# Optimization experiments

Measured on AMD Instinct MI355X. Metric: run time of the kernel, lower is better.

The kernel has to match this reference:

```python
import jax, jax.numpy as jnp
import numpy as np

M1, M2, BS = 2000, 400, 8
AT = M1 + M2
E1, E2, E3 = 60000, 20000, 20000
H, F, NG, L, C = 64, 64, 50, 4, 4
CUTOFF = 10.0
LOG2 = 0.6931471805599453  # shift of ShiftedSoftplus


def _ssp(x):
    return jax.nn.softplus(x) - LOG2


def _smear(d):
    # GaussianSmearing(0, cutoff, NG)
    offset = jnp.linspace(0.0, CUTOFF, NG)
    coeff = -0.5 / (offset[1] - offset[0]) ** 2
    return jnp.exp(coeff * (d[:, None] - offset[None, :]) ** 2)  # [E, NG]


def _colored_mlp(attr, colors, w1, b1, w2, b2):
    # w1:[C,NG,F] b1:[C,F] w2:[C,F,F] b2:[C,F]; route each edge through its color's MLP
    out = jnp.zeros((attr.shape[0], w1.shape[-1]), attr.dtype)
    for c in range(C):  # fixed small color count
        h = _ssp(attr @ w1[c] + b1[c]) @ w2[c] + b2[c]
        out = out + jnp.where((colors == c)[:, None], h, jnp.zeros((), attr.dtype))
    return out


def _block(h, ei, ew, attr, col, p):
    # InteractionBlock: CFConv -> ssp -> linear
    mw1, mb1, mw2, mb2, cw1, cw2, cb2, bw, bb = p
    Ccut = 0.5 * (jnp.cos(ew * jnp.pi / CUTOFF) + 1.0)
    W = _colored_mlp(attr, col, mw1, mb1, mw2, mb2) * Ccut[:, None]  # [E,F]
    x = h @ cw1                                   # lin1 (no bias) [N,F]
    msg = x[ei[:, 0]] * W                         # gather x_j, modulate
    agg = jax.ops.segment_sum(msg, ei[:, 1], num_segments=h.shape[0])  # scatter-add
    x = agg @ cw2 + cb2                           # lin2
    return _ssp(x) @ bw + bb                      # act + block linear


def _batch_graph(ei, ew, col):
    # replicate per-structure edges across the batch with node offset b*AT
    offs = (jnp.arange(BS, dtype=ei.dtype) * AT)[:, None, None]
    ei_b = (ei[None] + offs).reshape(-1, 2)
    return ei_b, jnp.tile(ew, BS), jnp.tile(col, BS)


def _forward(sites, sites_p, e1, ew1, c1, e2, ew2, c2, e3, ew3, c3,
             emb_w, emb_p_w, mlp_w1, mlp_b1, mlp_w2, mlp_b2,
             conv_w1, conv_w2, conv_b2, blk_w, blk_b,
             out_w1, out_b1, out_w2, out_b2):
    h = jnp.concatenate([emb_w[sites], emb_p_w[sites_p]], axis=1).reshape(BS * AT, H)
    graphs = []
    for (ei, ew, col) in ((e1, ew1, c1), (e2, ew2, c2), (e3, ew3, c3)):
        ei_b, ew_b, col_b = _batch_graph(ei, ew, col)
        graphs.append((ei_b, ew_b, col_b, _smear(ew_b)))
    for l in range(L):
        delta = jnp.zeros_like(h)
        for g, (ei_b, ew_b, col_b, attr_b) in enumerate(graphs):
            p = (mlp_w1[l, g], mlp_b1[l, g], mlp_w2[l, g], mlp_b2[l, g],
                 conv_w1[l, g], conv_w2[l, g], conv_b2[l, g], blk_w[l, g], blk_b[l, g])
            delta = delta + _block(h, ei_b, ew_b, attr_b, col_b, p)
        h = h + delta
    hp = h.reshape(BS, AT, H)[:, M1:, :]   # mask selects pore nodes only
    o = hp @ out_w1 + out_b1               # NB: original has `h - self.act(h)` no-op, so no activation here
    o = o @ out_w2 + out_b2                # [BS, M2, 1]
    return o.sum(axis=1)                   # 'add' readout per batch -> [BS, 1]


def setup_inputs() -> dict:
    key = jax.random.key(0)
    ks = jax.random.split(key, 24)
    f = lambda i, shape, s=0.1: jax.random.normal(ks[i], shape, jnp.float32) * s
    sites = jax.random.randint(ks[0], (BS, M1), 0, 1, dtype=jnp.int32)
    sites_p = jax.random.randint(ks[1], (BS, M2), 0, 2, dtype=jnp.int32)
    e1 = jax.random.randint(ks[2], (E1, 2), 0, M1, dtype=jnp.int32)
    e2 = jnp.stack([jax.random.randint(ks[3], (E2,), 0, M1, dtype=jnp.int32),
                    jax.random.randint(ks[4], (E2,), M1, AT, dtype=jnp.int32)], 1)
    e3 = jnp.stack([jax.random.randint(ks[5], (E3,), M1, AT, dtype=jnp.int32),
                    jax.random.randint(ks[6], (E3,), 0, M1, dtype=jnp.int32)], 1)
    ew1 = jax.random.uniform(ks[7], (E1,), jnp.float32, 0.5, CUTOFF)
    ew2 = jax.random.uniform(ks[8], (E2,), jnp.float32, 0.5, CUTOFF)
    ew3 = jax.random.uniform(ks[9], (E3,), jnp.float32, 0.5, CUTOFF)
    c1 = jax.random.randint(ks[10], (E1,), 0, C, dtype=jnp.int32)
    c2 = jax.random.randint(ks[11], (E2,), 0, C, dtype=jnp.int32)
    c3 = jax.random.randint(ks[12], (E3,), 0, C, dtype=jnp.int32)
    return {
        'sites': sites, 'sites_p': sites_p,
        'edge_idx1': e1, 'edge_weight1': ew1, 'colors1': c1,
        'edge_idx2': e2, 'edge_weight2': ew2, 'colors2': c2,
        'edge_idx3': e3, 'edge_weight3': ew3, 'colors3': c3,
        'emb_w': f(13, (1, H), 1.0), 'emb_p_w': f(14, (2, H), 1.0),
        'mlp_w1': f(15, (L, 3, C, NG, F)), 'mlp_b1': jnp.zeros((L, 3, C, F), jnp.float32),
        'mlp_w2': f(16, (L, 3, C, F, F)), 'mlp_b2': jnp.zeros((L, 3, C, F), jnp.float32),
        'conv_w1': f(17, (L, 3, H, F)), 'conv_w2': f(18, (L, 3, F, H)),
        'conv_b2': jnp.zeros((L, 3, H), jnp.float32),
        'blk_w': f(19, (L, 3, H, H)), 'blk_b': jnp.zeros((L, 3, H), jnp.float32),
        'out_w1': f(20, (H, H // 2)), 'out_b1': jnp.zeros((H // 2,), jnp.float32),
        'out_w2': f(21, (H // 2, 1)), 'out_b2': jnp.zeros((1,), jnp.float32),
    }


def reference(sites, sites_p, edge_idx1, edge_weight1, colors1,
              edge_idx2, edge_weight2, colors2, edge_idx3, edge_weight3, colors3,
              emb_w, emb_p_w, mlp_w1, mlp_b1, mlp_w2, mlp_b2,
              conv_w1, conv_w2, conv_b2, blk_w, blk_b,
              out_w1, out_b1, out_w2, out_b2):
    return _forward(sites, sites_p, edge_idx1, edge_weight1, colors1,
                    edge_idx2, edge_weight2, colors2, edge_idx3, edge_weight3, colors3,
                    emb_w, emb_p_w, mlp_w1, mlp_b1, mlp_w2, mlp_b2,
                    conv_w1, conv_w2, conv_b2, blk_w, blk_b,
                    out_w1, out_b1, out_w2, out_b2)
```

## Files before the change

### kernel.cpp

```cpp
#include <hip/hip_runtime.h>
#include <math.h>

constexpr int M1 = 2000, M2 = 400, BS = 8;
constexpr int AT = M1 + M2;
constexpr int NN = BS * AT;
constexpr int E1 = 60000, E2 = 20000, E3 = 20000;
constexpr int ET = E1 + E2 + E3;
constexpr int H = 64, F = 64, NG = 50, L = 4, C = 4;
constexpr float CUTOFF = 10.0f;
constexpr float LOG2F_ = 0.6931471805599453f;

constexpr float SMEAR_STEP = 10.0f / 49.0f;
constexpr float SMEAR_COEFF = -12.005f;
constexpr float PI_OVER_CUT = 0.31415926535897932f;

constexpr int NBLK = (ET + 255) / 256;

constexpr int NT = 256;
constexpr float DSCALE = (float)(NT - 1) / CUTOFF;

constexpr int TILE_M = 32;

constexpr int SITE_T = M1 / 4;
constexpr int PORE_T = M2 / 4;
constexpr int NTILE  = SITE_T + PORE_T;

constexpr int LT0 = M1 / 4;
constexpr int LT1 = M1 / 4;
constexpr int LT2 = M2 / 4;
constexpr int LTOT = LT0 + LT1 + LT2;

constexpr int A_TAB  = 48 * NT / 4;
constexpr int A_INIT = NN * 64 / 256;
constexpr int A_CNT  = NBLK;
constexpr int A_CV   = 3;
constexpr int A_TOT  = A_TAB + A_INIT + A_CNT + A_CV;
constexpr int B_PACK = 48 * NT * 64 / 256;
constexpr int B_TOT  = B_PACK + 3 + 2;

constexpr size_t O_HA    = 0;
constexpr size_t O_HB    = O_HA  + (size_t)NN * 64 * 4;
constexpr size_t O_XG    = O_HB  + (size_t)NN * 64 * 4;
constexpr size_t O_DG    = O_XG  + (size_t)3 * AT * 512 * 2;
constexpr size_t O_TAB2  = O_DG  + (size_t)3 * NN * 64 * 4;
constexpr size_t O_EDATA = O_TAB2 + (size_t)48 * NT * 64 * 4;
constexpr size_t O_INT   = O_EDATA + (size_t)ET * 16;
constexpr int I_DEG  = 0;
constexpr int I_CUR  = 7200;
constexpr int I_ZEND = 14400;
constexpr int I_BASE = 14400;
constexpr int I_PERM = 21616;
constexpr int I_CV   = 26016;

__device__ inline float sspf(float x) {
    return fmaxf(x, 0.0f) + log1pf(expf(-fabsf(x))) - LOG2F_;
}
__device__ inline float sspf_fast(float x) {
    float t = __expf(-fabsf(x));
    return fmaxf(x, 0.0f) + __logf(1.0f + t) - LOG2F_;
}

__device__ inline unsigned int bf16rn(float x) {
    unsigned int u = __float_as_uint(x);
    u = (u + 0x7FFFu + ((u >> 16) & 1u)) >> 16;
    return u & 0xFFFFu;
}

__device__ inline int graph_off(int g) { return g == 0 ? 0 : (g == 1 ? E1 : E1 + E2); }

__device__ inline void edge_decode(int idx, int& g, int& e,
                                   const int* ei1, const int* ei2, const int* ei3,
                                   const int* c1, const int* c2, const int* c3,
                                   const int*& ei, const int*& cl) {
    if (idx < E1)            { g = 0; e = idx;           ei = ei1; cl = c1; }
    else if (idx < E1 + E2)  { g = 1; e = idx - E1;      ei = ei2; cl = c2; }
    else                     { g = 2; e = idx - E1 - E2; ei = ei3; cl = c3; }
}

__global__ __launch_bounds__(256) void k_setupA(
    const float* __restrict__ mlp_w1, const float* __restrict__ mlp_b1,
    const float* __restrict__ mlp_w2, const float* __restrict__ mlp_b2,
    float* __restrict__ tabF,
    const int* __restrict__ sites, const int* __restrict__ sites_p,
    const float* __restrict__ emb_w, const float* __restrict__ emb_p_w,
    float* __restrict__ h,
    const int* __restrict__ ei1, const int* __restrict__ ei2,
    const int* __restrict__ ei3, const int* __restrict__ c1,
    const int* __restrict__ c2, const int* __restrict__ c3,
    int* __restrict__ deg,
    const float* __restrict__ conv_b2, const float* __restrict__ blk_w,
    const float* __restrict__ blk_b, float* __restrict__ cvbuf) {
    int bid = blockIdx.x;
    int t = threadIdx.x;
    if (bid < A_TAB) {
        const int lane = t & 63;
        int w = bid * 4 + (t >> 6);
        int s = w / NT;
        int p = w - s * NT;
        int l = s % L;
        int gc = s / L;
        int c = gc % C;
        int g = gc / C;
        float d = (float)p * (CUTOFF / (float)(NT - 1));
        size_t wb = (size_t)((l * 3 + g) * C + c);
        const float* w1 = mlp_w1 + wb * NG * F;
        const float* w2 = mlp_w2 + wb * F * F;
        float w1c[NG], w2c[F];
        #pragma unroll
        for (int k = 0; k < NG; k++) w1c[k] = w1[k * F + lane];
        #pragma unroll
        for (int k = 0; k < F; k++) w2c[k] = w2[k * F + lane];
        float b1c = mlp_b1[wb * F + lane];
        float b2c = mlp_b2[wb * F + lane];
        float dd = d - (float)lane * SMEAR_STEP;
        float av = (lane < NG) ? __expf(SMEAR_COEFF * dd * dd) : 0.0f;
        float acc = b1c;
        #pragma unroll
        for (int k = 0; k < NG; k++) acc = fmaf(__shfl(av, k), w1c[k], acc);
        float tt = sspf_fast(acc);
        float acc2 = b2c;
        #pragma unroll
        for (int j = 0; j < F; j++) acc2 = fmaf(__shfl(tt, j), w2c[j], acc2);
        float ccut = 0.5f * (__cosf(d * PI_OVER_CUT) + 1.0f);
        tabF[((size_t)s * NT + p) * 64 + lane] = acc2 * ccut;
    } else if (bid < A_TAB + A_INIT) {
        int idx = (bid - A_TAB) * 256 + t;
        int f = idx & 63;
        int n = idx >> 6;
        int b = n / AT;
        int i = n - b * AT;
        float v;
        if (i < M1) v = emb_w[sites[b * M1 + i] * H + f];
        else        v = emb_p_w[sites_p[b * M2 + (i - M1)] * H + f];
        h[idx] = v;
    } else if (bid < A_TAB + A_INIT + A_CNT) {
        int idx = (bid - A_TAB - A_INIT) * 256 + t;
        if (idx < ET) {
            int g, e; const int* ei; const int* cl;
            edge_decode(idx, g, e, ei1, ei2, ei3, c1, c2, c3, ei, cl);
            atomicAdd(&deg[g * AT + ei[2 * e + 1]], 1);
        }
    } else {
        int s = (bid - A_TAB - A_INIT - A_CNT) * 4 + (t >> 6);
        int lane = t & 63;
        if (s < 12) {
            float sl = sspf(conv_b2[s * 64 + lane]);
            const float* bw = blk_w + (size_t)s * 4096;
            float a = blk_b[s * 64 + lane];
            #pragma unroll 8
            for (int k = 0; k < 64; k++)
                a = fmaf(__shfl(sl, k), bw[k * 64 + lane], a);
            cvbuf[s * 64 + lane] = a;
        }
    }
}

__global__ __launch_bounds__(256) void k_setupB(
// ... 34 lines not shown
        int tb = lsum[t] - s;
        #pragma unroll
        for (int i = 0; i < CH; i++) {
            int idx = t * CH + i;
            if (idx < AT) base[g * (AT + 1) + idx] = tb + loc[i];
        }
        if (t == T - 1) base[g * (AT + 1) + AT] = lsum[T - 1];
    } else {
        __shared__ int hist[256];
        __shared__ int cur[256];
        int q = bid - B_PACK - 3;
        int cnt   = q ? M2 : M1;
        int obase = q ? M1 : 0;
        hist[t] = 0;
        __syncthreads();
        for (int i = t; i < cnt; i += 256) {
            int key = q ? deg[AT + M1 + i] : (deg[i] + deg[2 * AT + i]);
            atomicAdd(&hist[min(key, 255)], 1);
        }
        __syncthreads();
        if (t == 0) {
            int run = 0;
            for (int k = 0; k < 256; k++) { cur[k] = run; run += hist[k]; }
        }
        __syncthreads();
        for (int i = t; i < cnt; i += 256) {
            int key = q ? deg[AT + M1 + i] : (deg[i] + deg[2 * AT + i]);
            int pos = atomicAdd(&cur[min(key, 255)], 1);
            perm[obase + pos] = q ? (M1 + i) : i;
        }
    }
}

__global__ void k_fill(const int* __restrict__ ei1, const int* __restrict__ ei2,
                       const int* __restrict__ ei3, const int* __restrict__ c1,
                       const int* __restrict__ c2, const int* __restrict__ c3,
                       const float* __restrict__ ew1, const float* __restrict__ ew2,
                       const float* __restrict__ ew3,
                       const int* __restrict__ base, int* __restrict__ cur,
                       int4* __restrict__ edata) {
    int idx = blockIdx.x * blockDim.x + threadIdx.x;
    if (idx >= ET) return;
    int g, e; const int* ei; const int* cl;
    edge_decode(idx, g, e, ei1, ei2, ei3, c1, c2, c3, ei, cl);
    const float* ew = (g == 0) ? ew1 : (g == 1 ? ew2 : ew3);
    int dst = ei[2 * e + 1];
    int src = ei[2 * e];
    int p = base[g * (AT + 1) + dst] + atomicAdd(&cur[g * AT + dst], 1);
    float t = ew[e] * DSCALE;
    int i0 = min((int)t, NT - 2);
    float fr = t - (float)i0;
    int cb = cl[e] * (L * NT) + i0;
    edata[graph_off(g) + p] = make_int4(src, cb, __float_as_int(fr), 0);
}

__device__ inline void fma4(float acc[4], float a, const float4 b) {
    acc[0] = fmaf(a, b.x, acc[0]);
    acc[1] = fmaf(a, b.y, acc[1]);
    acc[2] = fmaf(a, b.z, acc[2]);
    acc[3] = fmaf(a, b.w, acc[3]);
}

__device__ inline void stage_B(const float* __restrict__ gB, float (*Bs)[68], int t) {
    #pragma unroll
    for (int i = 0; i < 4; i++) {
        int v = t + i * 256;
        int r = v >> 4, c4 = (v & 15) * 4;
        *(float4*)&Bs[r][c4] = *(const float4*)(gB + (size_t)r * 64 + c4);
    }
}
__device__ inline void gemm_tile(const float (*As)[68], const float (*Bs)[68],
                                 int r0, int c0, float acc0[4], float acc1[4]) {
    #pragma unroll 4
    for (int k0 = 0; k0 < 64; k0 += 4) {
        float4 a0 = *(const float4*)&As[r0][k0];
        float4 a1 = *(const float4*)&As[r0 + 1][k0];
        float4 b0 = *(const float4*)&Bs[k0][c0];
        float4 b1 = *(const float4*)&Bs[k0 + 1][c0];
        float4 b2 = *(const float4*)&Bs[k0 + 2][c0];
        float4 b3 = *(const float4*)&Bs[k0 + 3][c0];
        fma4(acc0, a0.x, b0); fma4(acc0, a0.y, b1);
        fma4(acc0, a0.z, b2); fma4(acc0, a0.w, b3);
        fma4(acc1, a1.x, b0); fma4(acc1, a1.y, b1);
        fma4(acc1, a1.z, b2); fma4(acc1, a1.w, b3);
    }
}

__device__ inline void xg_transpose_store(const float (*T)[68],
                                          unsigned short* __restrict__ xg,
                                          int g, int i0, int t) {
    int k = t >> 6, c = t & 63;
    unsigned int w0 = bf16rn(T[k * 8 + 0][c]) | (bf16rn(T[k * 8 + 1][c]) << 16);
    unsigned int w1 = bf16rn(T[k * 8 + 2][c]) | (bf16rn(T[k * 8 + 3][c]) << 16);
    unsigned int w2 = bf16rn(T[k * 8 + 4][c]) | (bf16rn(T[k * 8 + 5][c]) << 16);
    unsigned int w3 = bf16rn(T[k * 8 + 6][c]) | (bf16rn(T[k * 8 + 7][c]) << 16);
    unsigned short* out = xg + (((size_t)g * AT + i0 + k) * 64 + c) * 8;
    *(uint4*)out = make_uint4(w0, w1, w2, w3);
}

__device__ inline void xg_tstore(const float (*T)[68],
                                 unsigned short* __restrict__ xg,
                                 int g, const int* __restrict__ perm,
                                 int pbase, int gi, int t) {
    int k = t >> 6, c = t & 63;
    int node = perm[pbase + gi * 4 + k];
    unsigned int w0 = bf16rn(T[k * 8 + 0][c]) | (bf16rn(T[k * 8 + 1][c]) << 16);
    unsigned int w1 = bf16rn(T[k * 8 + 2][c]) | (bf16rn(T[k * 8 + 3][c]) << 16);
    unsigned int w2 = bf16rn(T[k * 8 + 4][c]) | (bf16rn(T[k * 8 + 5][c]) << 16);
    unsigned int w3 = bf16rn(T[k * 8 + 6][c]) | (bf16rn(T[k * 8 + 7][c]) << 16);
    unsigned short* out = xg + (((size_t)g * AT + node) * 64 + c) * 8;
    *(uint4*)out = make_uint4(w0, w1, w2, w3);
}

__device__ inline void lin1_map(int bid, int& g, int& igrp) {
    if (bid < LT0)            { g = 0; igrp = bid; }
    else if (bid < LT0 + LT1) { g = 1; igrp = bid - LT0; }
    else                      { g = 2; igrp = LT0 + (bid - LT0 - LT1); }
}

__global__ __launch_bounds__(256) void k_lin1t(
    const float* __restrict__ h, const float* __restrict__ conv_w1,
    unsigned short* __restrict__ xg, int l) {
    __shared__ float As[TILE_M][68];
    __shared__ float Bs[64][68];
    int t = threadIdx.x;
    int g, igrp;
    lin1_map(blockIdx.x, g, igrp);
    int i0 = igrp * 4;
    #pragma unroll
    for (int it = 0; it < 2; it++) {
        int v = t + it * 256;
        int r = v >> 4, c4 = (v & 15) * 4;
        int n = (r & 7) * AT + i0 + (r >> 3);
        *(float4*)&As[r][c4] = *(const float4*)(h + (size_t)n * 64 + c4);
    }
    stage_B(conv_w1 + (size_t)(l * 3 + g) * 4096, Bs, t);
    __syncthreads();
    int cg = t & 15, rg = t >> 4;
    int c0 = cg * 4, r0 = rg * 2;
    float acc0[4] = {0, 0, 0, 0}, acc1[4] = {0, 0, 0, 0};
    gemm_tile(As, Bs, r0, c0, acc0, acc1);
    __syncthreads();
    *(float4*)&As[r0][c0]     = make_float4(acc0[0], acc0[1], acc0[2], acc0[3]);
    *(float4*)&As[r0 + 1][c0] = make_float4(acc1[0], acc1[1], acc1[2], acc1[3]);
    __syncthreads();
    xg_transpose_store(As, xg, g, i0, t);
}

__device__ inline void gather_dst(const int4* __restrict__ ed, int s, int e,
                                  const unsigned int* __restrict__ tg,
                                  const unsigned short* __restrict__ xgg,
                                  int lane, float acc[8]) {
    int i = s;
    while (i < e) {
        int cnt = min(e - i, 64);
        int4 mrec = ed[i + min(lane, cnt - 1)];
        int j = 0;
        for (; j + 2 <= cnt; j += 2) {
            int x0 = __shfl(mrec.x, j),     y0 = __shfl(mrec.y, j),     z0 = __shfl(mrec.z, j);
            int x1 = __shfl(mrec.x, j + 1), y1 = __shfl(mrec.y, j + 1), z1 = __shfl(mrec.z, j + 1);
            unsigned int u0 = tg[(size_t)y0 * 64 + lane];
            unsigned int u1 = tg[(size_t)y1 * 64 + lane];
            uint4 q0 = *(const uint4*)(xgg + ((size_t)x0 * 64 + lane) * 8);
            uint4 q1 = *(const uint4*)(xgg + ((size_t)x1 * 64 + lane) * 8);
            float lo0 = __uint_as_float(u0 << 16);
            float hi0 = __uint_as_float(u0 & 0xFFFF0000u);
            float lo1 = __uint_as_float(u1 << 16);
            float hi1 = __uint_as_float(u1 & 0xFFFF0000u);
            float wl0 = fmaf(__int_as_float(z0), hi0 - lo0, lo0);
            float wl1 = fmaf(__int_as_float(z1), hi1 - lo1, lo1);
            acc[0] = fmaf(__uint_as_float(q0.x << 16),         wl0, acc[0]);
            acc[1] = fmaf(__uint_as_float(q0.x & 0xFFFF0000u), wl0, acc[1]);
            acc[2] = fmaf(__uint_as_float(q0.y << 16),         wl0, acc[2]);
            acc[3] = fmaf(__uint_as_float(q0.y & 0xFFFF0000u), wl0, acc[3]);
            acc[4] = fmaf(__uint_as_float(q0.z << 16),         wl0, acc[4]);
            acc[5] = fmaf(__uint_as_float(q0.z & 0xFFFF0000u), wl0, acc[5]);
            acc[6] = fmaf(__uint_as_float(q0.w << 16),         wl0, acc[6]);
            acc[7] = fmaf(__uint_as_float(q0.w & 0xFFFF0000u), wl0, acc[7]);
            acc[0] = fmaf(__uint_as_float(q1.x << 16),         wl1, acc[0]);
            acc[1] = fmaf(__uint_as_float(q1.x & 0xFFFF0000u), wl1, acc[1]);
            acc[2] = fmaf(__uint_as_float(q1.y << 16),         wl1, acc[2]);
            acc[3] = fmaf(__uint_as_float(q1.y & 0xFFFF0000u), wl1, acc[3]);
            acc[4] = fmaf(__uint_as_float(q1.z << 16),         wl1, acc[4]);
            acc[5] = fmaf(__uint_as_float(q1.z & 0xFFFF0000u), wl1, acc[5]);
            acc[6] = fmaf(__uint_as_float(q1.w << 16),         wl1, acc[6]);
            acc[7] = fmaf(__uint_as_float(q1.w & 0xFFFF0000u), wl1, acc[7]);
        }
        if (j < cnt) {
            int x0 = __shfl(mrec.x, j), y0 = __shfl(mrec.y, j), z0 = __shfl(mrec.z, j);
            unsigned int u0 = tg[(size_t)y0 * 64 + lane];
            uint4 q = *(const uint4*)(xgg + ((size_t)x0 * 64 + lane) * 8);
            float lo0 = __uint_as_float(u0 << 16);
            float hi0 = __uint_as_float(u0 & 0xFFFF0000u);
            float wl = fmaf(__int_as_float(z0), hi0 - lo0, lo0);
            acc[0] = fmaf(__uint_as_float(q.x << 16),         wl, acc[0]);
            acc[1] = fmaf(__uint_as_float(q.x & 0xFFFF0000u), wl, acc[1]);
            acc[2] = fmaf(__uint_as_float(q.y << 16),         wl, acc[2]);
            acc[3] = fmaf(__uint_as_float(q.y & 0xFFFF0000u), wl, acc[3]);
            acc[4] = fmaf(__uint_as_float(q.z << 16),         wl, acc[4]);
            acc[5] = fmaf(__uint_as_float(q.z & 0xFFFF0000u), wl, acc[5]);
            acc[6] = fmaf(__uint_as_float(q.w << 16),         wl, acc[6]);
            acc[7] = fmaf(__uint_as_float(q.w & 0xFFFF0000u), wl, acc[7]);
        }
        i += cnt;
    }
}

__global__ __launch_bounds__(256) void k_layer(
    const int4* __restrict__ edata, const int* __restrict__ base,
    const int* __restrict__ perm,
    unsigned short* __restrict__ xg, const unsigned int* __restrict__ tab2,
    const float* __restrict__ conv_w2, const float* __restrict__ conv_b2,
    const float* __restrict__ blk_w, const float* __restrict__ blk_b,
    const float* __restrict__ conv_w1, const float* __restrict__ cvbuf,
    const float* __restrict__ hIn, float* __restrict__ hOut,
    int l, int last) {
    __shared__ float As[TILE_M][68];
    __shared__ float Bs[64][68];
    int t = threadIdx.x;
    const int lane = t & 63;
    const int wv = t >> 6;
    int bid = blockIdx.x;
    int site = (bid < SITE_T) ? 1 : 0;
    int gi = site ? (SITE_T - 1 - bid) : (PORE_T - 1 - (bid - SITE_T));
    int pbperm = site ? 0 : M1;
    int gA = site ? 0 : 1;
    int dst = perm[pbperm + gi * 4 + wv];
    size_t pbA = (size_t)(l * 3 + gA);
    stage_B(conv_w2 + pbA * 4096, Bs, t);

    float accA[8], accB[8];
    #pragma unroll
    for (int j = 0; j < 8; j++) { accA[j] = 0.0f; accB[j] = 0.0f; }
    {
        int s = base[gA * (AT + 1) + dst];
        int e = base[gA * (AT + 1) + dst + 1];
        gather_dst(edata + graph_off(gA), s, e,
                   tab2 + ((size_t)gA * C * L + l) * NT * 64,
                   xg + (size_t)gA * AT * 512, lane, accA);
    }
    if (site) {
        int s = base[2 * (AT + 1) + dst];
        int e = base[2 * (AT + 1) + dst + 1];
        gather_dst(edata + graph_off(2), s, e,
                   tab2 + ((size_t)2 * C * L + l) * NT * 64,
                   xg + (size_t)2 * AT * 512, lane, accB);
    }
    #pragma unroll
    for (int b = 0; b < 8; b++) As[wv * 8 + b][lane] = accA[b];
    __syncthreads();

    int cg = t & 15, rg = t >> 4;
    int c0 = cg * 4, r0 = rg * 2;
    float4 cbA = *(const float4*)(conv_b2 + pbA * 64 + c0);
    float x0[4] = {cbA.x, cbA.y, cbA.z, cbA.w};
    float x1[4] = {cbA.x, cbA.y, cbA.z, cbA.w};
    gemm_tile(As, Bs, r0, c0, x0, x1);
    __syncthreads();
    *(float4*)&As[r0][c0] =
        make_float4(sspf(x0[0]), sspf(x0[1]), sspf(x0[2]), sspf(x0[3]));
    *(float4*)&As[r0 + 1][c0] =
        make_float4(sspf(x1[0]), sspf(x1[1]), sspf(x1[2]), sspf(x1[3]));
    stage_B(blk_w + pbA * 4096, Bs, t);
    __syncthreads();

    int kk = r0 >> 3, b0 = r0 & 7;
    int nodek = perm[pbperm + gi * 4 + kk];
    size_t o0 = ((size_t)b0 * AT + nodek) * 64 + c0;
    size_t o1 = o0 + (size_t)AT * 64;
    float4 h0 = *(const float4*)(hIn + o0);
    float4 h1 = *(const float4*)(hIn + o1);
    const float* cvl = cvbuf + (size_t)l * 3 * 64;
    float4 bbA = *(const float4*)(blk_b + pbA * 64 + c0);
    float4 ex;
    if (site) {
        float4 bbB = *(const float4*)(blk_b + (size_t)(l * 3 + 2) * 64 + c0);
        float4 c1v = *(const float4*)(cvl + 64 + c0);
        ex = make_float4(bbB.x + c1v.x, bbB.y + c1v.y, bbB.z + c1v.z, bbB.w + c1v.w);
    } else {
        float4 c0v = *(const float4*)(cvl + c0);
        float4 c2v = *(const float4*)(cvl + 128 + c0);
        ex = make_float4(c0v.x + c2v.x, c0v.y + c2v.y, c0v.z + c2v.z, c0v.w + c2v.w);
    }
    float d0[4] = {h0.x + bbA.x + ex.x, h0.y + bbA.y + ex.y,
                   h0.z + bbA.z + ex.z, h0.w + bbA.w + ex.w};
    float d1[4] = {h1.x + bbA.x + ex.x, h1.y + bbA.y + ex.y,
                   h1.z + bbA.z + ex.z, h1.w + bbA.w + ex.w};
    gemm_tile(As, Bs, r0, c0, d0, d1);

    if (site) {
        __syncthreads();
        #pragma unroll
        for (int b = 0; b < 8; b++) As[wv * 8 + b][lane] = accB[b];
        stage_B(conv_w2 + (size_t)(l * 3 + 2) * 4096, Bs, t);
        __syncthreads();
        float4 cbB = *(const float4*)(conv_b2 + (size_t)(l * 3 + 2) * 64 + c0);
        float y0[4] = {cbB.x, cbB.y, cbB.z, cbB.w};
        float y1[4] = {cbB.x, cbB.y, cbB.z, cbB.w};
        gemm_tile(As, Bs, r0, c0, y0, y1);
        __syncthreads();
        *(float4*)&As[r0][c0] =
            make_float4(sspf(y0[0]), sspf(y0[1]), sspf(y0[2]), sspf(y0[3]));
        *(float4*)&As[r0 + 1][c0] =
            make_float4(sspf(y1[0]), sspf(y1[1]), sspf(y1[2]), sspf(y1[3]));
        stage_B(blk_w + (size_t)(l * 3 + 2) * 4096, Bs, t);
        __syncthreads();
        gemm_tile(As, Bs, r0, c0, d0, d1);
    }

    *(float4*)(hOut + o0) = make_float4(d0[0], d0[1], d0[2], d0[3]);
    *(float4*)(hOut + o1) = make_float4(d1[0], d1[1], d1[2], d1[3]);
    if (last) return;

    __syncthreads();
    *(float4*)&As[r0][c0]     = make_float4(d0[0], d0[1], d0[2], d0[3]);
    *(float4*)&As[r0 + 1][c0] = make_float4(d1[0], d1[1], d1[2], d1[3]);
    int gB = site ? 0 : 2;
    stage_B(conv_w1 + (size_t)((l + 1) * 3 + gB) * 4096, Bs, t);
    __syncthreads();
    float p0[4] = {0, 0, 0, 0}, p1[4] = {0, 0, 0, 0};
    gemm_tile(As, Bs, r0, c0, p0, p1);
    if (site) {
        __syncthreads();
        stage_B(conv_w1 + (size_t)((l + 1) * 3 + 1) * 4096, Bs, t);
        __syncthreads();
        float q0[4] = {0, 0, 0, 0}, q1[4] = {0, 0, 0, 0};
        gemm_tile(As, Bs, r0, c0, q0, q1);
        __syncthreads();
        *(float4*)&As[r0][c0]     = make_float4(p0[0], p0[1], p0[2], p0[3]);
        *(float4*)&As[r0 + 1][c0] = make_float4(p1[0], p1[1], p1[2], p1[3]);
        *(float4*)&Bs[r0][c0]     = make_float4(q0[0], q0[1], q0[2], q0[3]);
        *(float4*)&Bs[r0 + 1][c0] = make_float4(q1[0], q1[1], q1[2], q1[3]);
        __syncthreads();
        xg_tstore(As, xg, 0, perm, pbperm, gi, t);
        xg_tstore((const float(*)[68])Bs, xg, 1, perm, pbperm, gi, t);
    } else {
        __syncthreads();
        *(float4*)&As[r0][c0]     = make_float4(p0[0], p0[1], p0[2], p0[3]);
        *(float4*)&As[r0 + 1][c0] = make_float4(p1[0], p1[1], p1[2], p1[3]);
        __syncthreads();
        xg_tstore(As, xg, 2, perm, pbperm, gi, t);
    }
}

__global__ void k_read(const float* __restrict__ h,
                       const float* __restrict__ w1, const float* __restrict__ b1,
                       const float* __restrict__ w2, const float* __restrict__ b2,
                       float* __restrict__ out) {
    int b = blockIdx.x;
    int lane = threadIdx.x & 63;
    int wv = threadIdx.x >> 6;
    __shared__ float part[4];
    float weff = 0.0f;
    #pragma unroll
    for (int j = 0; j < H / 2; j++) weff = fmaf(w1[lane * (H / 2) + j], w2[j], weff);
    float acc = 0.0f;
    for (int i = wv * (M2 / 4); i < (wv + 1) * (M2 / 4); i++)
        acc += h[((size_t)b * AT + M1 + i) * H + lane];
    float v = acc * weff;
    for (int off = 32; off; off >>= 1) v += __shfl_xor(v, off);
    if (lane == 0) part[wv] = v;
    __syncthreads();
    if (threadIdx.x == 0) {
        float bias = b2[0];
        for (int j = 0; j < H / 2; j++) bias = fmaf(b1[j], w2[j], bias);
        out[b] = part[0] + part[1] + part[2] + part[3] + (float)M2 * bias;
    }
}

extern "C" void kernel_launch(void* const* d_in, const int* in_sizes, int n_in,
                              void* d_out, int out_size, void* d_ws, size_t ws_size,
                              hipStream_t stream) {
    const int* sites   = (const int*)d_in[0];
    const int* sites_p = (const int*)d_in[1];
    const int* ei1 = (const int*)d_in[2];
// ... 12 lines not shown
    const float* mlp_w2 = (const float*)d_in[15];
    const float* mlp_b2 = (const float*)d_in[16];
    const float* conv_w1 = (const float*)d_in[17];
    const float* conv_w2 = (const float*)d_in[18];
    const float* conv_b2 = (const float*)d_in[19];
    const float* blk_w = (const float*)d_in[20];
    const float* blk_b = (const float*)d_in[21];
    const float* out_w1 = (const float*)d_in[22];
    const float* out_b1 = (const float*)d_in[23];
    const float* out_w2 = (const float*)d_in[24];
    const float* out_b2 = (const float*)d_in[25];

    char* ws = (char*)d_ws;
    float* hA   = (float*)(ws + O_HA);
    float* hB   = (float*)(ws + O_HB);
    unsigned short* xg = (unsigned short*)(ws + O_XG);
    float* tabF = (float*)(ws + O_DG);
    unsigned int* tab2 = (unsigned int*)(ws + O_TAB2);
    int4*  edata = (int4*)(ws + O_EDATA);
    int* ip    = (int*)(ws + O_INT);
    int* deg   = ip + I_DEG;
    int* cur   = ip + I_CUR;
    int* ibase = ip + I_BASE;
    int* dperm = ip + I_PERM;
    float* cvbuf = (float*)(ip + I_CV);

    hipMemsetAsync(ip, 0, (size_t)I_ZEND * sizeof(int), stream);

    k_setupA<<<A_TOT, 256, 0, stream>>>(mlp_w1, mlp_b1, mlp_w2, mlp_b2, tabF,
                                        sites, sites_p, emb_w, emb_p_w, hA,
                                        ei1, ei2, ei3, c1, c2, c3, deg,
                                        conv_b2, blk_w, blk_b, cvbuf);
    k_setupB<<<B_TOT, 256, 0, stream>>>(tabF, tab2, deg, ibase, dperm);
    k_fill<<<NBLK, 256, 0, stream>>>(ei1, ei2, ei3, c1, c2, c3, ew1, ew2, ew3,
                                     ibase, cur, edata);

    k_lin1t<<<LTOT, 256, 0, stream>>>(hA, conv_w1, xg, 0);
    float* hcur = hA;
    float* hnxt = hB;
    for (int l = 0; l < L; l++) {
        int last = (l == L - 1) ? 1 : 0;
        k_layer<<<NTILE, 256, 0, stream>>>(edata, ibase, dperm, xg, tab2,
                                           conv_w2, conv_b2, blk_w, blk_b,
                                           conv_w1, cvbuf, hcur, hnxt, l, last);
        float* tmp = hcur; hcur = hnxt; hnxt = tmp;
    }
    k_read<<<BS, 256, 0, stream>>>(hcur, out_w1, out_b1, out_w2, out_b2, (float*)d_out);
}
```

Before: 323.1 us.

## Split layer blocks by batch half, fuse fill with lin1, batch table build

Each layer kernel's per-node tile is split into two blocks, each covering four of the eight batch copies. The xg layout is repacked so every half stores 4 bf16 values per feature, and the gather loop is unrolled to four edges. The edge fill and the first lin1 kernel are merged into one launch, saving a dispatch. Table setup now has each wave compute 16 table points so the MLP weights loaded into registers are reused. The change doubles the gather index and table traffic per node, traded for more parallelism and smaller per-block work.

```diff
diff --git a/kernel.cpp b/kernel.cpp
--- a/kernel.cpp
+++ b/kernel.cpp
@@ -23,14 +23,14 @@
 
 constexpr int SITE_T = M1 / 4;
 constexpr int PORE_T = M2 / 4;
-constexpr int NTILE  = SITE_T + PORE_T;
+constexpr int NBLK_L = 2 * (SITE_T + PORE_T);
 
 constexpr int LT0 = M1 / 4;
 constexpr int LT1 = M1 / 4;
 constexpr int LT2 = M2 / 4;
 constexpr int LTOT = LT0 + LT1 + LT2;
 
-constexpr int A_TAB  = 48 * NT / 4;
+constexpr int A_TAB  = 192;
 constexpr int A_INIT = NN * 64 / 256;
 constexpr int A_CNT  = NBLK;
 constexpr int A_CV   = 3;
@@ -94,14 +94,13 @@
     int t = threadIdx.x;
     if (bid < A_TAB) {
         const int lane = t & 63;
-        int w = bid * 4 + (t >> 6);
-        int s = w / NT;
-        int p = w - s * NT;
+        int wslot = bid * 4 + (t >> 6);
+        int s = wslot >> 4;
+        int pq = wslot & 15;
         int l = s % L;
         int gc = s / L;
         int c = gc % C;
         int g = gc / C;
-        float d = (float)p * (CUTOFF / (float)(NT - 1));
         size_t wb = (size_t)((l * 3 + g) * C + c);
         const float* w1 = mlp_w1 + wb * NG * F;
         const float* w2 = mlp_w2 + wb * F * F;
@@ -112,17 +111,21 @@
         for (int k = 0; k < F; k++) w2c[k] = w2[k * F + lane];
         float b1c = mlp_b1[wb * F + lane];
         float b2c = mlp_b2[wb * F + lane];
-        float dd = d - (float)lane * SMEAR_STEP;
-        float av = (lane < NG) ? __expf(SMEAR_COEFF * dd * dd) : 0.0f;
-        float acc = b1c;
-        #pragma unroll
-        for (int k = 0; k < NG; k++) acc = fmaf(__shfl(av, k), w1c[k], acc);
-        float tt = sspf_fast(acc);
-        float acc2 = b2c;
-        #pragma unroll
-        for (int j = 0; j < F; j++) acc2 = fmaf(__shfl(tt, j), w2c[j], acc2);
-        float ccut = 0.5f * (__cosf(d * PI_OVER_CUT) + 1.0f);
-        tabF[((size_t)s * NT + p) * 64 + lane] = acc2 * ccut;
+        for (int pp = 0; pp < 16; pp++) {
+            int p = pq * 16 + pp;
+            float d = (float)p * (CUTOFF / (float)(NT - 1));
+            float dd = d - (float)lane * SMEAR_STEP;
+            float av = (lane < NG) ? __expf(SMEAR_COEFF * dd * dd) : 0.0f;
+            float acc = b1c;
+            #pragma unroll
+            for (int k = 0; k < NG; k++) acc = fmaf(__shfl(av, k), w1c[k], acc);
+            float tt = sspf_fast(acc);
+            float acc2 = b2c;
+            #pragma unroll
+            for (int j = 0; j < F; j++) acc2 = fmaf(__shfl(tt, j), w2c[j], acc2);
+            float ccut = 0.5f * (__cosf(d * PI_OVER_CUT) + 1.0f);
+            tabF[((size_t)s * NT + p) * 64 + lane] = acc2 * ccut;
+        }
     } else if (bid < A_TAB + A_INIT) {
         int idx = (bid - A_TAB) * 256 + t;
         int f = idx & 63;
@@ -223,28 +226,6 @@
     }
 }
 
-__global__ void k_fill(const int* __restrict__ ei1, const int* __restrict__ ei2,
-                       const int* __restrict__ ei3, const int* __restrict__ c1,
-                       const int* __restrict__ c2, const int* __restrict__ c3,
-                       const float* __restrict__ ew1, const float* __restrict__ ew2,
-                       const float* __restrict__ ew3,
-                       const int* __restrict__ base, int* __restrict__ cur,
-                       int4* __restrict__ edata) {
-    int idx = blockIdx.x * blockDim.x + threadIdx.x;
-    if (idx >= ET) return;
-    int g, e; const int* ei; const int* cl;
-    edge_decode(idx, g, e, ei1, ei2, ei3, c1, c2, c3, ei, cl);
-    const float* ew = (g == 0) ? ew1 : (g == 1 ? ew2 : ew3);
-    int dst = ei[2 * e + 1];
-    int src = ei[2 * e];
-    int p = base[g * (AT + 1) + dst] + atomicAdd(&cur[g * AT + dst], 1);
-    float t = ew[e] * DSCALE;
-    int i0 = min((int)t, NT - 2);
-    float fr = t - (float)i0;
-    int cb = cl[e] * (L * NT) + i0;
-    edata[graph_off(g) + p] = make_int4(src, cb, __float_as_int(fr), 0);
-}
-
 __device__ inline void fma4(float acc[4], float a, const float4 b) {
     acc[0] = fmaf(a, b.x, acc[0]);
     acc[1] = fmaf(a, b.y, acc[1]);
@@ -276,122 +257,91 @@
         fma4(acc1, a1.z, b2); fma4(acc1, a1.w, b3);
     }
 }
-
-__device__ inline void xg_transpose_store(const float (*T)[68],
-                                          unsigned short* __restrict__ xg,
-                                          int g, int i0, int t) {
+__device__ inline void gemm_row(const float (*As)[68], const float (*Bs)[68],
+                                int r, int c0, float acc[4]) {
+    #pragma unroll 4
+    for (int k0 = 0; k0 < 64; k0 += 4) {
+        float4 a = *(const float4*)&As[r][k0];
+        float4 b0 = *(const float4*)&Bs[k0][c0];
+        float4 b1 = *(const float4*)&Bs[k0 + 1][c0];
+        float4 b2 = *(const float4*)&Bs[k0 + 2][c0];
+        float4 b3 = *(const float4*)&Bs[k0 + 3][c0];
+        fma4(acc, a.x, b0); fma4(acc, a.y, b1);
+        fma4(acc, a.z, b2); fma4(acc, a.w, b3);
+    }
+}
+
+__device__ inline void xg_store8(const float (*T)[68],
+                                 unsigned short* __restrict__ xg,
+                                 int g, int i0, int t) {
     int k = t >> 6, c = t & 63;
     unsigned int w0 = bf16rn(T[k * 8 + 0][c]) | (bf16rn(T[k * 8 + 1][c]) << 16);
     unsigned int w1 = bf16rn(T[k * 8 + 2][c]) | (bf16rn(T[k * 8 + 3][c]) << 16);
     unsigned int w2 = bf16rn(T[k * 8 + 4][c]) | (bf16rn(T[k * 8 + 5][c]) << 16);
     unsigned int w3 = bf16rn(T[k * 8 + 6][c]) | (bf16rn(T[k * 8 + 7][c]) << 16);
-    unsigned short* out = xg + (((size_t)g * AT + i0 + k) * 64 + c) * 8;
-    *(uint4*)out = make_uint4(w0, w1, w2, w3);
-}
-
-__device__ inline void xg_tstore(const float (*T)[68],
+    unsigned short* o0 = xg + (((size_t)(g * 2 + 0) * AT + i0 + k) * 64 + c) * 4;
+    unsigned short* o1 = xg + (((size_t)(g * 2 + 1) * AT + i0 + k) * 64 + c) * 4;
+    *(uint2*)o0 = make_uint2(w0, w1);
+    *(uint2*)o1 = make_uint2(w2, w3);
+}
+__device__ inline void xg_store4(const float (*T)[68],
                                  unsigned short* __restrict__ xg,
-                                 int g, const int* __restrict__ perm,
+                                 int g, int bh, const int* __restrict__ perm,
                                  int pbase, int gi, int t) {
     int k = t >> 6, c = t & 63;
     int node = perm[pbase + gi * 4 + k];
-    unsigned int w0 = bf16rn(T[k * 8 + 0][c]) | (bf16rn(T[k * 8 + 1][c]) << 16);
-    unsigned int w1 = bf16rn(T[k * 8 + 2][c]) | (bf16rn(T[k * 8 + 3][c]) << 16);
-    unsigned int w2 = bf16rn(T[k * 8 + 4][c]) | (bf16rn(T[k * 8 + 5][c]) << 16);
-    unsigned int w3 = bf16rn(T[k * 8 + 6][c]) | (bf16rn(T[k * 8 + 7][c]) << 16);
-    unsigned short* out = xg + (((size_t)g * AT + node) * 64 + c) * 8;
-    *(uint4*)out = make_uint4(w0, w1, w2, w3);
-}
-
-__device__ inline void lin1_map(int bid, int& g, int& igrp) {
-    if (bid < LT0)            { g = 0; igrp = bid; }
-    else if (bid < LT0 + LT1) { g = 1; igrp = bid - LT0; }
-    else                      { g = 2; igrp = LT0 + (bid - LT0 - LT1); }
-}
-
-__global__ __launch_bounds__(256) void k_lin1t(
-    const float* __restrict__ h, const float* __restrict__ conv_w1,
-    unsigned short* __restrict__ xg, int l) {
-    __shared__ float As[TILE_M][68];
-    __shared__ float Bs[64][68];
-    int t = threadIdx.x;
-    int g, igrp;
-    lin1_map(blockIdx.x, g, igrp);
-    int i0 = igrp * 4;
-    #pragma unroll
-    for (int it = 0; it < 2; it++) {
-        int v = t + it * 256;
-        int r = v >> 4, c4 = (v & 15) * 4;
-        int n = (r & 7) * AT + i0 + (r >> 3);
-        *(float4*)&As[r][c4] = *(const float4*)(h + (size_t)n * 64 + c4);
-    }
-    stage_B(conv_w1 + (size_t)(l * 3 + g) * 4096, Bs, t);
-    __syncthreads();
-    int cg = t & 15, rg = t >> 4;
-    int c0 = cg * 4, r0 = rg * 2;
-    float acc0[4] = {0, 0, 0, 0}, acc1[4] = {0, 0, 0, 0};
-    gemm_tile(As, Bs, r0, c0, acc0, acc1);
-    __syncthreads();
-    *(float4*)&As[r0][c0]     = make_float4(acc0[0], acc0[1], acc0[2], acc0[3]);
-    *(float4*)&As[r0 + 1][c0] = make_float4(acc1[0], acc1[1], acc1[2], acc1[3]);
-    __syncthreads();
-    xg_transpose_store(As, xg, g, i0, t);
-}
-
-__device__ inline void gather_dst(const int4* __restrict__ ed, int s, int e,
-                                  const unsigned int* __restrict__ tg,
-                                  const unsigned short* __restrict__ xgg,
-                                  int lane, float acc[8]) {
+    unsigned int w0 = bf16rn(T[k * 4 + 0][c]) | (bf16rn(T[k * 4 + 1][c]) << 16);
+    unsigned int w1 = bf16rn(T[k * 4 + 2][c]) | (bf16rn(T[k * 4 + 3][c]) << 16);
+    unsigned short* out = xg + (((size_t)(g * 2 + bh) * AT + node) * 64 + c) * 4;
+    *(uint2*)out = make_uint2(w0, w1);
+}
+
+__device__ inline float tab_lerp(unsigned int u, int z) {
+    float lo = __uint_as_float(u << 16);
+    float hi = __uint_as_float(u & 0xFFFF0000u);
+    return fmaf(__int_as_float(z), hi - lo, lo);
+}
+__device__ inline void gmadd(float acc[4], uint2 q, float wl) {
+    acc[0] = fmaf(__uint_as_float(q.x << 16),         wl, acc[0]);
+    acc[1] = fmaf(__uint_as_float(q.x & 0xFFFF0000u), wl, acc[1]);
+    acc[2] = fmaf(__uint_as_float(q.y << 16),         wl, acc[2]);
+    acc[3] = fmaf(__uint_as_float(q.y & 0xFFFF0000u), wl, acc[3]);
+}
+
+__device__ inline void gather4(const int4* __restrict__ ed, int s, int e,
+                               const unsigned int* __restrict__ tg,
+                               const unsigned short* __restrict__ xgg,
+                               int lane, float acc[4]) {
     int i = s;
     while (i < e) {
         int cnt = min(e - i, 64);
         int4 mrec = ed[i + min(lane, cnt - 1)];
         int j = 0;
-        for (; j + 2 <= cnt; j += 2) {
+        for (; j + 4 <= cnt; j += 4) {
             int x0 = __shfl(mrec.x, j),     y0 = __shfl(mrec.y, j),     z0 = __shfl(mrec.z, j);
             int x1 = __shfl(mrec.x, j + 1), y1 = __shfl(mrec.y, j + 1), z1 = __shfl(mrec.z, j + 1);
+            int x2 = __shfl(mrec.x, j + 2), y2 = __shfl(mrec.y, j + 2), z2 = __shfl(mrec.z, j + 2);
+            int x3 = __shfl(mrec.x, j + 3), y3 = __shfl(mrec.y, j + 3), z3 = __shfl(mrec.z, j + 3);
             unsigned int u0 = tg[(size_t)y0 * 64 + lane];
             unsigned int u1 = tg[(size_t)y1 * 64 + lane];
-            uint4 q0 = *(const uint4*)(xgg + ((size_t)x0 * 64 + lane) * 8);
-            uint4 q1 = *(const uint4*)(xgg + ((size_t)x1 * 64 + lane) * 8);
-            float lo0 = __uint_as_float(u0 << 16);
-            float hi0 = __uint_as_float(u0 & 0xFFFF0000u);
-            float lo1 = __uint_as_float(u1 << 16);
-            float hi1 = __uint_as_float(u1 & 0xFFFF0000u);
-            float wl0 = fmaf(__int_as_float(z0), hi0 - lo0, lo0);
-            float wl1 = fmaf(__int_as_float(z1), hi1 - lo1, lo1);
-            acc[0] = fmaf(__uint_as_float(q0.x << 16),         wl0, acc[0]);
-            acc[1] = fmaf(__uint_as_float(q0.x & 0xFFFF0000u), wl0, acc[1]);
-            acc[2] = fmaf(__uint_as_float(q0.y << 16),         wl0, acc[2]);
-            acc[3] = fmaf(__uint_as_float(q0.y & 0xFFFF0000u), wl0, acc[3]);
-            acc[4] = fmaf(__uint_as_float(q0.z << 16),         wl0, acc[4]);
-            acc[5] = fmaf(__uint_as_float(q0.z & 0xFFFF0000u), wl0, acc[5]);
-            acc[6] = fmaf(__uint_as_float(q0.w << 16),         wl0, acc[6]);
-            acc[7] = fmaf(__uint_as_float(q0.w & 0xFFFF0000u), wl0, acc[7]);
-            acc[0] = fmaf(__uint_as_float(q1.x << 16),         wl1, acc[0]);
-            acc[1] = fmaf(__uint_as_float(q1.x & 0xFFFF0000u), wl1, acc[1]);
-            acc[2] = fmaf(__uint_as_float(q1.y << 16),         wl1, acc[2]);
-            acc[3] = fmaf(__uint_as_float(q1.y & 0xFFFF0000u), wl1, acc[3]);
-            acc[4] = fmaf(__uint_as_float(q1.z << 16),         wl1, acc[4]);
-            acc[5] = fmaf(__uint_as_float(q1.z & 0xFFFF0000u), wl1, acc[5]);
-            acc[6] = fmaf(__uint_as_float(q1.w << 16),         wl1, acc[6]);
-            acc[7] = fmaf(__uint_as_float(q1.w & 0xFFFF0000u), wl1, acc[7]);
-        }
-        if (j < cnt) {
+            unsigned int u2 = tg[(size_t)y2 * 64 + lane];
+            unsigned int u3 = tg[(size_t)y3 * 64 + lane];
+            uint2 q0 = *(const uint2*)(xgg + ((size_t)x0 << 8) + lane * 4);
+            uint2 q1 = *(const uint2*)(xgg + ((size_t)x1 << 8) + lane * 4);
+            uint2 q2 = *(const uint2*)(xgg + ((size_t)x2 << 8) + lane * 4);
+            uint2 q3 = *(const uint2*)(xgg + ((size_t)x3 << 8) + lane * 4);
+            float wl0 = tab_lerp(u0, z0);
+            float wl1 = tab_lerp(u1, z1);
+            float wl2 = tab_lerp(u2, z2);
+            float wl3 = tab_lerp(u3, z3);
+            gmadd(acc, q0, wl0); gmadd(acc, q1, wl1);
+            gmadd(acc, q2, wl2); gmadd(acc, q3, wl3);
+        }
+        for (; j < cnt; j++) {
             int x0 = __shfl(mrec.x, j), y0 = __shfl(mrec.y, j), z0 = __shfl(mrec.z, j);
             unsigned int u0 = tg[(size_t)y0 * 64 + lane];
-            uint4 q = *(const uint4*)(xgg + ((size_t)x0 * 64 + lane) * 8);
-            float lo0 = __uint_as_float(u0 << 16);
-            float hi0 = __uint_as_float(u0 & 0xFFFF0000u);
-            float wl = fmaf(__int_as_float(z0), hi0 - lo0, lo0);
-            acc[0] = fmaf(__uint_as_float(q.x << 16),         wl, acc[0]);
-            acc[1] = fmaf(__uint_as_float(q.x & 0xFFFF0000u), wl, acc[1]);
-            acc[2] = fmaf(__uint_as_float(q.y << 16),         wl, acc[2]);
-            acc[3] = fmaf(__uint_as_float(q.y & 0xFFFF0000u), wl, acc[3]);
-            acc[4] = fmaf(__uint_as_float(q.z << 16),         wl, acc[4]);
-            acc[5] = fmaf(__uint_as_float(q.z & 0xFFFF0000u), wl, acc[5]);
-            acc[6] = fmaf(__uint_as_float(q.w << 16),         wl, acc[6]);
-            acc[7] = fmaf(__uint_as_float(q.w & 0xFFFF0000u), wl, acc[7]);
+            uint2 q0 = *(const uint2*)(xgg + ((size_t)x0 << 8) + lane * 4);
+            gmadd(acc, q0, tab_lerp(u0, z0));
         }
         i += cnt;
     }
@@ -406,132 +356,175 @@
     const float* __restrict__ conv_w1, const float* __restrict__ cvbuf,
     const float* __restrict__ hIn, float* __restrict__ hOut,
     int l, int last) {
+    __shared__ float As[16][68];
+    __shared__ float Ps[16][68];
+    __shared__ float Bs[64][68];
+    const int t = threadIdx.x;
+    const int lane = t & 63;
+    const int wv = t >> 6;
+    int bid = blockIdx.x;
+    int site, tile, bh;
+    if (bid < 2 * SITE_T) { site = 1; tile = bid >> 1; bh = bid & 1; }
+    else { site = 0; tile = (bid - 2 * SITE_T) >> 1; bh = (bid - 2 * SITE_T) & 1; }
+    const int gi = site ? (SITE_T - 1 - tile) : (PORE_T - 1 - tile);
+    const int pbperm = site ? 0 : M1;
+    const int gA = site ? 0 : 1;
+    const size_t pbA = (size_t)(l * 3 + gA);
+    const size_t pbB = (size_t)(l * 3 + 2);
+
+    stage_B(conv_w2 + pbA * 4096, Bs, t);
+
+    const int dst = perm[pbperm + gi * 4 + wv];
+    float accA[4] = {0, 0, 0, 0}, accB[4] = {0, 0, 0, 0};
+    {
+        int s = base[gA * (AT + 1) + dst];
+        int e = base[gA * (AT + 1) + dst + 1];
+        gather4(edata + graph_off(gA), s, e,
+                tab2 + ((size_t)gA * C * L + l) * NT * 64,
+                xg + (size_t)(gA * 2 + bh) * AT * 256, lane, accA);
+    }
+    if (site) {
+        int s = base[2 * (AT + 1) + dst];
+        int e = base[2 * (AT + 1) + dst + 1];
+        gather4(edata + graph_off(2), s, e,
+                tab2 + ((size_t)2 * C * L + l) * NT * 64,
+                xg + (size_t)(2 * 2 + bh) * AT * 256, lane, accB);
+    }
+    #pragma unroll
+    for (int b = 0; b < 4; b++) As[wv * 4 + b][lane] = accA[b];
+    __syncthreads();
+
+    const int r = t >> 4;
+    const int c0 = (t & 15) * 4;
+    const int k = r >> 2, bl = r & 3;
+    const int node = perm[pbperm + gi * 4 + k];
+    const int batch = bh * 4 + bl;
+    const size_t o = ((size_t)batch * AT + node) * 64 + c0;
+    const float* cvl = cvbuf + (size_t)l * 3 * 64;
+
+    float4 cb = *(const float4*)(conv_b2 + pbA * 64 + c0);
+    float x[4] = {cb.x, cb.y, cb.z, cb.w};
+    gemm_row(As, Bs, r, c0, x);
+    __syncthreads();
+    *(float4*)&As[r][c0] =
+        make_float4(sspf(x[0]), sspf(x[1]), sspf(x[2]), sspf(x[3]));
+    stage_B(blk_w + pbA * 4096, Bs, t);
+    __syncthreads();
+
+    float4 hv = *(const float4*)(hIn + o);
+    float4 bbA = *(const float4*)(blk_b + pbA * 64 + c0);
+    float d[4];
+    if (site) {
+        float4 bbB = *(const float4*)(blk_b + pbB * 64 + c0);
+        float4 cv1 = *(const float4*)(cvl + 64 + c0);
+        d[0] = hv.x + bbA.x + bbB.x + cv1.x;
+        d[1] = hv.y + bbA.y + bbB.y + cv1.y;
+        d[2] = hv.z + bbA.z + bbB.z + cv1.z;
+        d[3] = hv.w + bbA.w + bbB.w + cv1.w;
+    } else {
+        float4 cv0 = *(const float4*)(cvl + c0);
+        float4 cv2 = *(const float4*)(cvl + 128 + c0);
+        d[0] = hv.x + bbA.x + cv0.x + cv2.x;
+        d[1] = hv.y + bbA.y + cv0.y + cv2.y;
+        d[2] = hv.z + bbA.z + cv0.z + cv2.z;
+        d[3] = hv.w + bbA.w + cv0.w + cv2.w;
+    }
+    gemm_row(As, Bs, r, c0, d);
+    if (site) {
+        __syncthreads();
+        #pragma unroll
+        for (int b = 0; b < 4; b++) As[wv * 4 + b][lane] = accB[b];
+        stage_B(conv_w2 + pbB * 4096, Bs, t);
+        __syncthreads();
+        float4 cb2v = *(const float4*)(conv_b2 + pbB * 64 + c0);
+        float y[4] = {cb2v.x, cb2v.y, cb2v.z, cb2v.w};
+        gemm_row(As, Bs, r, c0, y);
+        __syncthreads();
+        *(float4*)&As[r][c0] =
+            make_float4(sspf(y[0]), sspf(y[1]), sspf(y[2]), sspf(y[3]));
+        stage_B(blk_w + pbB * 4096, Bs, t);
+        __syncthreads();
+        gemm_row(As, Bs, r, c0, d);
+    }
+    *(float4*)(hOut + o) = make_float4(d[0], d[1], d[2], d[3]);
+    if (last) return;
+
+    __syncthreads();
+    *(float4*)&As[r][c0] = make_float4(d[0], d[1], d[2], d[3]);
+    stage_B(conv_w1 + (size_t)((l + 1) * 3 + (site ? 0 : 2)) * 4096, Bs, t);
+    __syncthreads();
+    float p[4] = {0, 0, 0, 0};
+    gemm_row(As, Bs, r, c0, p);
+    __syncthreads();
+    *(float4*)&Ps[r][c0] = make_float4(p[0], p[1], p[2], p[3]);
+    if (site) stage_B(conv_w1 + (size_t)((l + 1) * 3 + 1) * 4096, Bs, t);
+    __syncthreads();
+    xg_store4(Ps, xg, site ? 0 : 2, bh, perm, pbperm, gi, t);
+    if (site) {
+        float q[4] = {0, 0, 0, 0};
+        gemm_row(As, Bs, r, c0, q);
+        __syncthreads();
+        *(float4*)&Ps[r][c0] = make_float4(q[0], q[1], q[2], q[3]);
+        __syncthreads();
+        xg_store4(Ps, xg, 1, bh, perm, pbperm, gi, t);
+    }
+}
+
+__global__ __launch_bounds__(256) void k_fl(
+    const int* __restrict__ ei1, const int* __restrict__ ei2,
+    const int* __restrict__ ei3, const int* __restrict__ c1,
+    const int* __restrict__ c2, const int* __restrict__ c3,
+    const float* __restrict__ ew1, const float* __restrict__ ew2,
+    const float* __restrict__ ew3,
+    const int* __restrict__ base, int* __restrict__ cur,
+    int4* __restrict__ edata,
+    const float* __restrict__ h, const float* __restrict__ conv_w1,
+    unsigned short* __restrict__ xg) {
     __shared__ float As[TILE_M][68];
     __shared__ float Bs[64][68];
     int t = threadIdx.x;
-    const int lane = t & 63;
-    const int wv = t >> 6;
-    int bid = blockIdx.x;
-    int site = (bid < SITE_T) ? 1 : 0;
-    int gi = site ? (SITE_T - 1 - bid) : (PORE_T - 1 - (bid - SITE_T));
-    int pbperm = site ? 0 : M1;
-    int gA = site ? 0 : 1;
-    int dst = perm[pbperm + gi * 4 + wv];
-    size_t pbA = (size_t)(l * 3 + gA);
-    stage_B(conv_w2 + pbA * 4096, Bs, t);
-
-    float accA[8], accB[8];
+    if (blockIdx.x >= LTOT) {
+        int idx = (blockIdx.x - LTOT) * 256 + t;
+        if (idx >= ET) return;
+        int g, e; const int* ei; const int* cl;
+        edge_decode(idx, g, e, ei1, ei2, ei3, c1, c2, c3, ei, cl);
+        const float* ew = (g == 0) ? ew1 : (g == 1 ? ew2 : ew3);
+        int dst = ei[2 * e + 1];
+        int src = ei[2 * e];
+        int p = base[g * (AT + 1) + dst] + atomicAdd(&cur[g * AT + dst], 1);
+        float tt = ew[e] * DSCALE;
+        int i0 = min((int)tt, NT - 2);
+        float fr = tt - (float)i0;
+        int cb = cl[e] * (L * NT) + i0;
+        edata[graph_off(g) + p] = make_int4(src, cb, __float_as_int(fr), 0);
+        return;
+    }
+    int g, igrp;
+    {
+        int bid = blockIdx.x;
+        if (bid < LT0)            { g = 0; igrp = bid; }
+        else if (bid < LT0 + LT1) { g = 1; igrp = bid - LT0; }
+        else                      { g = 2; igrp = LT0 + (bid - LT0 - LT1); }
+    }
+    int i0 = igrp * 4;
     #pragma unroll
-    for (int j = 0; j < 8; j++) { accA[j] = 0.0f; accB[j] = 0.0f; }
-    {
-        int s = base[gA * (AT + 1) + dst];
-        int e = base[gA * (AT + 1) + dst + 1];
-        gather_dst(edata + graph_off(gA), s, e,
-                   tab2 + ((size_t)gA * C * L + l) * NT * 64,
-                   xg + (size_t)gA * AT * 512, lane, accA);
-    }
-    if (site) {
-        int s = base[2 * (AT + 1) + dst];
-        int e = base[2 * (AT + 1) + dst + 1];
-        gather_dst(edata + graph_off(2), s, e,
-                   tab2 + ((size_t)2 * C * L + l) * NT * 64,
-                   xg + (size_t)2 * AT * 512, lane, accB);
-    }
-    #pragma unroll
-    for (int b = 0; b < 8; b++) As[wv * 8 + b][lane] = accA[b];
-    __syncthreads();
-
+    for (int it = 0; it < 2; it++) {
+        int v = t + it * 256;
+        int r = v >> 4, c4 = (v & 15) * 4;
+        int n = (r & 7) * AT + i0 + (r >> 3);
+        *(float4*)&As[r][c4] = *(const float4*)(h + (size_t)n * 64 + c4);
+    }
+    stage_B(conv_w1 + (size_t)g * 4096, Bs, t);
+    __syncthreads();
     int cg = t & 15, rg = t >> 4;
     int c0 = cg * 4, r0 = rg * 2;
-    float4 cbA = *(const float4*)(conv_b2 + pbA * 64 + c0);
-    float x0[4] = {cbA.x, cbA.y, cbA.z, cbA.w};
-    float x1[4] = {cbA.x, cbA.y, cbA.z, cbA.w};
-    gemm_tile(As, Bs, r0, c0, x0, x1);
-    __syncthreads();
-    *(float4*)&As[r0][c0] =
-        make_float4(sspf(x0[0]), sspf(x0[1]), sspf(x0[2]), sspf(x0[3]));
-    *(float4*)&As[r0 + 1][c0] =
-        make_float4(sspf(x1[0]), sspf(x1[1]), sspf(x1[2]), sspf(x1[3]));
-    stage_B(blk_w + pbA * 4096, Bs, t);
-    __syncthreads();
-
-    int kk = r0 >> 3, b0 = r0 & 7;
-    int nodek = perm[pbperm + gi * 4 + kk];
-    size_t o0 = ((size_t)b0 * AT + nodek) * 64 + c0;
-    size_t o1 = o0 + (size_t)AT * 64;
-    float4 h0 = *(const float4*)(hIn + o0);
-    float4 h1 = *(const float4*)(hIn + o1);
-    const float* cvl = cvbuf + (size_t)l * 3 * 64;
-    float4 bbA = *(const float4*)(blk_b + pbA * 64 + c0);
-    float4 ex;
-    if (site) {
-        float4 bbB = *(const float4*)(blk_b + (size_t)(l * 3 + 2) * 64 + c0);
-        float4 c1v = *(const float4*)(cvl + 64 + c0);
-        ex = make_float4(bbB.x + c1v.x, bbB.y + c1v.y, bbB.z + c1v.z, bbB.w + c1v.w);
-    } else {
-        float4 c0v = *(const float4*)(cvl + c0);
-        float4 c2v = *(const float4*)(cvl + 128 + c0);
-        ex = make_float4(c0v.x + c2v.x, c0v.y + c2v.y, c0v.z + c2v.z, c0v.w + c2v.w);
-    }
-    float d0[4] = {h0.x + bbA.x + ex.x, h0.y + bbA.y + ex.y,
-                   h0.z + bbA.z + ex.z, h0.w + bbA.w + ex.w};
-    float d1[4] = {h1.x + bbA.x + ex.x, h1.y + bbA.y + ex.y,
-                   h1.z + bbA.z + ex.z, h1.w + bbA.w + ex.w};
-    gemm_tile(As, Bs, r0, c0, d0, d1);
-
-    if (site) {
-        __syncthreads();
-        #pragma unroll
-        for (int b = 0; b < 8; b++) As[wv * 8 + b][lane] = accB[b];
-        stage_B(conv_w2 + (size_t)(l * 3 + 2) * 4096, Bs, t);
-        __syncthreads();
-        float4 cbB = *(const float4*)(conv_b2 + (size_t)(l * 3 + 2) * 64 + c0);
-        float y0[4] = {cbB.x, cbB.y, cbB.z, cbB.w};
-        float y1[4] = {cbB.x, cbB.y, cbB.z, cbB.w};
-        gemm_tile(As, Bs, r0, c0, y0, y1);
-        __syncthreads();
-        *(float4*)&As[r0][c0] =
-            make_float4(sspf(y0[0]), sspf(y0[1]), sspf(y0[2]), sspf(y0[3]));
-        *(float4*)&As[r0 + 1][c0] =
-            make_float4(sspf(y1[0]), sspf(y1[1]), sspf(y1[2]), sspf(y1[3]));
-        stage_B(blk_w + (size_t)(l * 3 + 2) * 4096, Bs, t);
-        __syncthreads();
-        gemm_tile(As, Bs, r0, c0, d0, d1);
-    }
-
-    *(float4*)(hOut + o0) = make_float4(d0[0], d0[1], d0[2], d0[3]);
-    *(float4*)(hOut + o1) = make_float4(d1[0], d1[1], d1[2], d1[3]);
-    if (last) return;
-
-    __syncthreads();
-    *(float4*)&As[r0][c0]     = make_float4(d0[0], d0[1], d0[2], d0[3]);
-    *(float4*)&As[r0 + 1][c0] = make_float4(d1[0], d1[1], d1[2], d1[3]);
-    int gB = site ? 0 : 2;
-    stage_B(conv_w1 + (size_t)((l + 1) * 3 + gB) * 4096, Bs, t);
-    __syncthreads();
-    float p0[4] = {0, 0, 0, 0}, p1[4] = {0, 0, 0, 0};
-    gemm_tile(As, Bs, r0, c0, p0, p1);
-    if (site) {
-        __syncthreads();
-        stage_B(conv_w1 + (size_t)((l + 1) * 3 + 1) * 4096, Bs, t);
-        __syncthreads();
-        float q0[4] = {0, 0, 0, 0}, q1[4] = {0, 0, 0, 0};
-        gemm_tile(As, Bs, r0, c0, q0, q1);
-        __syncthreads();
-        *(float4*)&As[r0][c0]     = make_float4(p0[0], p0[1], p0[2], p0[3]);
-        *(float4*)&As[r0 + 1][c0] = make_float4(p1[0], p1[1], p1[2], p1[3]);
-        *(float4*)&Bs[r0][c0]     = make_float4(q0[0], q0[1], q0[2], q0[3]);
-        *(float4*)&Bs[r0 + 1][c0] = make_float4(q1[0], q1[1], q1[2], q1[3]);
-        __syncthreads();
-        xg_tstore(As, xg, 0, perm, pbperm, gi, t);
-        xg_tstore((const float(*)[68])Bs, xg, 1, perm, pbperm, gi, t);
-    } else {
-        __syncthreads();
-        *(float4*)&As[r0][c0]     = make_float4(p0[0], p0[1], p0[2], p0[3]);
-        *(float4*)&As[r0 + 1][c0] = make_float4(p1[0], p1[1], p1[2], p1[3]);
-        __syncthreads();
-        xg_tstore(As, xg, 2, perm, pbperm, gi, t);
-    }
+    float acc0[4] = {0, 0, 0, 0}, acc1[4] = {0, 0, 0, 0};
+    gemm_tile(As, Bs, r0, c0, acc0, acc1);
+    __syncthreads();
+    *(float4*)&As[r0][c0]     = make_float4(acc0[0], acc0[1], acc0[2], acc0[3]);
+    *(float4*)&As[r0 + 1][c0] = make_float4(acc1[0], acc1[1], acc1[2], acc1[3]);
+    __syncthreads();
+    xg_store8(As, xg, g, i0, t);
 }
 
 __global__ void k_read(const float* __restrict__ h,
@@ -610,17 +603,17 @@
                                         ei1, ei2, ei3, c1, c2, c3, deg,
                                         conv_b2, blk_w, blk_b, cvbuf);
     k_setupB<<<B_TOT, 256, 0, stream>>>(tabF, tab2, deg, ibase, dperm);
-    k_fill<<<NBLK, 256, 0, stream>>>(ei1, ei2, ei3, c1, c2, c3, ew1, ew2, ew3,
-                                     ibase, cur, edata);
-
-    k_lin1t<<<LTOT, 256, 0, stream>>>(hA, conv_w1, xg, 0);
+    k_fl<<<LTOT + NBLK, 256, 0, stream>>>(ei1, ei2, ei3, c1, c2, c3,
+                                          ew1, ew2, ew3, ibase, cur, edata,
+                                          hA, conv_w1, xg);
+
     float* hcur = hA;
     float* hnxt = hB;
     for (int l = 0; l < L; l++) {
         int last = (l == L - 1) ? 1 : 0;
-        k_layer<<<NTILE, 256, 0, stream>>>(edata, ibase, dperm, xg, tab2,
-                                           conv_w2, conv_b2, blk_w, blk_b,
-                                           conv_w1, cvbuf, hcur, hnxt, l, last);
+        k_layer<<<NBLK_L, 256, 0, stream>>>(edata, ibase, dperm, xg, tab2,
+                                            conv_w2, conv_b2, blk_w, blk_b,
+                                            conv_w1, cvbuf, hcur, hnxt, l, last);
         float* tmp = hcur; hcur = hnxt; hnxt = tmp;
     }
     k_read<<<BS, 256, 0, stream>>>(hcur, out_w1, out_b1, out_w2, out_b2, (float*)d_out);
```

Result: no change. 323.6 us (+0.2%).
